# Performance work log

Measured on AMD Instinct MI355X. Metric: run time of the kernel, lower is better.

## Reference

```python
import jax, jax.numpy as jnp
import numpy as np

LN_EPS = 1e-5

def _ln(x, w, b):
    mu = jnp.mean(x, -1, keepdims=True)
    var = jnp.mean((x - mu) ** 2, -1, keepdims=True)
    return (x - mu) / jnp.sqrt(var + LN_EPS) * w + b

def _rot_fwd(x, c, s):
    dh = x.shape[-1] // 2
    r, i = x[..., :dh], x[..., dh:]
    return jnp.concatenate([r * c - i * s, r * s + i * c], axis=-1)

def _rot_inv(x, c, s):
    dh = x.shape[-1] // 2
    r, i = x[..., :dh], x[..., dh:]
    return jnp.concatenate([r * c + i * s, -r * s + i * c], axis=-1)

def _sheaf(x, thetas, alpha, corr_W):
    # causal offsets for window=3
    B, T, d = x.shape
    offsets = [-3, -2, -1, 0]
    lap = jnp.zeros_like(x)
    for idx, delta in enumerate(offsets):
        th = thetas[idx]
        c, s = jnp.cos(th), jnp.sin(th)
        Rx = _rot_fwd(x, c, s)
        if delta == 0:
            x_nb = x
        else:
            ad = -delta
            zeros = jnp.zeros((B, ad, d), dtype=x.dtype)
            x_nb = jnp.concatenate([zeros, x[:, :T - ad, :]], axis=1)
        lap = lap + _rot_inv(Rx - x_nb, c, s)
    out = x - jnp.abs(alpha) * lap
    return out + jnp.einsum('btd,od->bto', out, corr_W)

def _gist_rotation(x, gist_theta, gist_mag, gist_weights, gist_strength, ln_w, ln_b):
    # Scale-1 path: gist_weights present. theta: (B, dh)
    dh = x.shape[-1] // 2
    w = gist_weights[..., None] * gist_mag              # (B, K, 1)
    w = w / (jnp.sum(w, axis=1, keepdims=True) + 1e-8)
    theta = jnp.sum(w * gist_theta, axis=1)             # (B, dh)
    theta = theta * jax.nn.sigmoid(gist_strength)
    c = jnp.cos(theta)[:, None, :]                      # (B, 1, dh)
    s = jnp.sin(theta)[:, None, :]
    r, i = x[..., :dh], x[..., dh:]
    rot = jnp.concatenate([r * c - i * s, r * s + i * c], axis=-1)
    return _ln(rot, ln_w, ln_b)

def _gist_cross_attn(x, gist_theta, gist_mag, Wq, Wk, Wv, Wo, gist_up_W, gist_up_b, n_heads=16):
    B, T, d = x.shape
    K = gist_theta.shape[1]
    dh = d // n_heads
    gist_repr = jnp.einsum('bkf,of->bko', jnp.concatenate([gist_theta, gist_mag], axis=-1), gist_up_W) + gist_up_b  # (B,K,d)
    Q = jnp.einsum('btd,od->bto', x, Wq).reshape(B, T, n_heads, dh).transpose(0, 2, 1, 3)          # (B,H,T,dh)
    Kh = jnp.einsum('bkd,od->bko', gist_repr, Wk).reshape(B, K, n_heads, dh).transpose(0, 2, 1, 3)  # (B,H,K,dh)
    V = jnp.einsum('bkd,od->bko', gist_repr, Wv).reshape(B, K, n_heads, dh).transpose(0, 2, 1, 3)
    scores = jnp.einsum('bhtd,bhkd->bhtk', Q, Kh) / jnp.sqrt(jnp.asarray(dh, x.dtype))
    ctx = jnp.einsum('bhtk,bhkd->bhtd', jax.nn.softmax(scores, axis=-1), V)
    ctx = ctx.transpose(0, 2, 1, 3).reshape(B, T, d)
    return jnp.einsum('btd,od->bto', ctx, Wo)

def _forward(x, gist_theta, gist_mag, gist_weights,
             ln_sheaf_w, ln_sheaf_b, sheaf_thetas, alpha, corr_W,
             ln_gist_w, ln_gist_b, gist_strength, gr_ln_w, gr_ln_b,
             ln_gca_w, ln_gca_b, Wq, Wk, Wv, Wo, gist_up_W, gist_up_b):
    x = x + _sheaf(_ln(x, ln_sheaf_w, ln_sheaf_b), sheaf_thetas, alpha, corr_W)
    xn = _ln(x, ln_gist_w, ln_gist_b)
    x = x + (_gist_rotation(xn, gist_theta, gist_mag, gist_weights, gist_strength, gr_ln_w, gr_ln_b) - xn)
    x = x + _gist_cross_attn(_ln(x, ln_gca_w, ln_gca_b), gist_theta, gist_mag,
                             Wq, Wk, Wv, Wo, gist_up_W, gist_up_b)
    return x

def setup_inputs() -> dict:
    key = jax.random.key(0)
    ks = jax.random.split(key, 16)
    B, T, d, K = 4, 2048, 2048, 16
    dh = d // 2
    scale = 1.0 / np.sqrt(d)
    inp = {
        'x': jax.random.normal(ks[0], (B, T, d), jnp.float32),
        'gist_theta': jax.random.normal(ks[1], (B, K, dh), jnp.float32),
        'gist_mag': jax.random.uniform(ks[2], (B, K, 1), jnp.float32),
        'gist_weights': jax.random.uniform(ks[3], (B, K), jnp.float32),
        'ln_sheaf_w': jnp.ones((d,), jnp.float32),
        'ln_sheaf_b': jnp.zeros((d,), jnp.float32),
        'sheaf_thetas': 0.1 * jax.random.normal(ks[4], (4, dh), jnp.float32),
        'alpha': jnp.asarray(0.15, jnp.float32),
        'corr_W': scale * jax.random.normal(ks[5], (d, d), jnp.float32),
        'ln_gist_w': jnp.ones((d,), jnp.float32),
        'ln_gist_b': jnp.zeros((d,), jnp.float32),
        'gist_strength': jnp.asarray(0.0, jnp.float32),
        'gr_ln_w': jnp.ones((d,), jnp.float32),
        'gr_ln_b': jnp.zeros((d,), jnp.float32),
        'ln_gca_w': jnp.ones((d,), jnp.float32),
        'ln_gca_b': jnp.zeros((d,), jnp.float32),
        'Wq': scale * jax.random.normal(ks[6], (d, d), jnp.float32),
        'Wk': scale * jax.random.normal(ks[7], (d, d), jnp.float32),
        'Wv': scale * jax.random.normal(ks[8], (d, d), jnp.float32),
        'Wo': scale * jax.random.normal(ks[9], (d, d), jnp.float32),
        'gist_up_W': (1.0 / np.sqrt(dh + 1)) * jax.random.normal(ks[10], (d, dh + 1), jnp.float32),
        'gist_up_b': jnp.zeros((d,), jnp.float32),
    }
    return inp

def reference(x, gist_theta, gist_mag, gist_weights,
              ln_sheaf_w, ln_sheaf_b, sheaf_thetas, alpha, corr_W,
              ln_gist_w, ln_gist_b, gist_strength, gr_ln_w, gr_ln_b,
              ln_gca_w, ln_gca_b, Wq, Wk, Wv, Wo, gist_up_W, gist_up_b):
    return _forward(x, gist_theta, gist_mag, gist_weights,
                    ln_sheaf_w, ln_sheaf_b, sheaf_thetas, alpha, corr_W,
                    ln_gist_w, ln_gist_b, gist_strength, gr_ln_w, gr_ln_b,
                    ln_gca_w, ln_gca_b, Wq, Wk, Wv, Wo, gist_up_W, gist_up_b)
```

## Files before the change

kernel.cpp:

```cpp
#include <hip/hip_runtime.h>
#include <hip/hip_bf16.h>

typedef unsigned short u16;
typedef unsigned int   u32;

using frag_ab = __attribute__((ext_vector_type(8))) short;
using frag_cd = __attribute__((ext_vector_type(4))) float;

__device__ __forceinline__ float bf2f(u16 u) {
    union { u32 i; float f; } v; v.i = ((u32)u) << 16; return v.f;
}
__device__ __forceinline__ u16 f2bf(float f) {
    __hip_bfloat16 h = __float2bfloat16(f);
    u16 u; __builtin_memcpy(&u, &h, 2); return u;
}
__device__ __forceinline__ float lo2f(u32 u) { union { u32 i; float f; } v; v.i = u << 16; return v.f; }
__device__ __forceinline__ float hi2f(u32 u) { union { u32 i; float f; } v; v.i = u & 0xffff0000u; return v.f; }
__device__ __forceinline__ void unpack8(uint4 v, float* f) {
    f[0]=lo2f(v.x); f[1]=hi2f(v.x); f[2]=lo2f(v.y); f[3]=hi2f(v.y);
    f[4]=lo2f(v.z); f[5]=hi2f(v.z); f[6]=lo2f(v.w); f[7]=hi2f(v.w);
}
__device__ __forceinline__ void load4f(const u16* p, float* f) {
    ushort4 v = *reinterpret_cast<const ushort4*>(p);
    f[0]=bf2f(v.x); f[1]=bf2f(v.y); f[2]=bf2f(v.z); f[3]=bf2f(v.w);
}
__device__ __forceinline__ void store4bf(u16* p, const float* f) {
    ushort4 v; v.x=f2bf(f[0]); v.y=f2bf(f[1]); v.z=f2bf(f[2]); v.w=f2bf(f[3]);
    *reinterpret_cast<ushort4*>(p) = v;
}
__device__ __forceinline__ u32 pack2(float a, float b) {
    return (u32)f2bf(a) | ((u32)f2bf(b) << 16);
}

__device__ __forceinline__ void gld16(const u16* g, u16* l) {
    __builtin_amdgcn_global_load_lds(
        (const __attribute__((address_space(1))) u32*)g,
        (__attribute__((address_space(3))) u32*)l, 16, 0, 0);
}

__device__ __forceinline__ u32 ldsaddr(const u16* p) {
    return (u32)(uintptr_t)(const __attribute__((address_space(3))) u16*)p;
}

__device__ __forceinline__ frag_ab dsread16(u32 a) {
    frag_ab r;
    asm volatile("ds_read_b128 %0, %1" : "=v"(r) : "v"(a));
    return r;
}

__device__ __forceinline__ void block_reduce2(float& s, float& ss, float* red) {
    #pragma unroll
    for (int off = 32; off > 0; off >>= 1) {
        s  += __shfl_down(s, off, 64);
        ss += __shfl_down(ss, off, 64);
    }
    int wv = threadIdx.x >> 6, ln = threadIdx.x & 63;
    if (ln == 0) { red[wv*2] = s; red[wv*2+1] = ss; }
    __syncthreads();
    s  = red[0] + red[2] + red[4] + red[6];
    ss = red[1] + red[3] + red[5] + red[7];
    __syncthreads();
}

__global__ __launch_bounds__(256) void convert_kernel(
    const float* __restrict__ in, u16* __restrict__ out, int n4)
{
    int i = blockIdx.x * 256 + threadIdx.x;
    if (i < n4) {
        float4 v = reinterpret_cast<const float4*>(in)[i];
        ushort4 o; o.x=f2bf(v.x); o.y=f2bf(v.y); o.z=f2bf(v.z); o.w=f2bf(v.w);
        reinterpret_cast<ushort4*>(out)[i] = o;
    }
}

__global__ __launch_bounds__(256) void convert2_kernel(
    const float* __restrict__ s0, const float* __restrict__ s1,
    u16* __restrict__ d0, u16* __restrict__ d1, int n4)
{
    int i = blockIdx.x * 256 + threadIdx.x;
    if (i >= n4) return;
    const float* s = blockIdx.y ? s1 : s0;
    u16*         d = blockIdx.y ? d1 : d0;
    float4 v = reinterpret_cast<const float4*>(s)[i];
    ushort4 o; o.x=f2bf(v.x); o.y=f2bf(v.y); o.z=f2bf(v.z); o.w=f2bf(v.w);
    reinterpret_cast<ushort4*>(d)[i] = o;
}

__global__ __launch_bounds__(256) void convert3_kernel(
    const float* __restrict__ s0, const float* __restrict__ s1,
    const float* __restrict__ s2,
    u16* __restrict__ d0, u16* __restrict__ d1, u16* __restrict__ d2, int n4)
{
    int i = blockIdx.x * 256 + threadIdx.x;
    if (i >= n4) return;
    const float* s = blockIdx.y == 0 ? s0 : (blockIdx.y == 1 ? s1 : s2);
    u16*         d = blockIdx.y == 0 ? d0 : (blockIdx.y == 1 ? d1 : d2);
    float4 v = reinterpret_cast<const float4*>(s)[i];
    ushort4 o; o.x=f2bf(v.x); o.y=f2bf(v.y); o.z=f2bf(v.z); o.w=f2bf(v.w);
    reinterpret_cast<ushort4*>(d)[i] = o;
}

__global__ __launch_bounds__(256) void apad_kernel(
    const float* __restrict__ gth, const float* __restrict__ gmag,
    u16* __restrict__ Abuf)
{
    const int r = blockIdx.x;
    const int tid = threadIdx.x;
    for (int c0 = tid*4; c0 < 1056; c0 += 1024) {
        float f[4];
        #pragma unroll
        for (int i = 0; i < 4; ++i) {
            int c = c0 + i;
            f[i] = (c < 1024) ? gth[(size_t)r*1024 + c] : (c == 1024 ? gmag[r] : 0.f);
        }
        store4bf(Abuf + (size_t)r*1056 + c0, f);
    }
}

__global__ __launch_bounds__(256) void wpad_kernel(
    const float* __restrict__ upW, u16* __restrict__ Bbuf)
{
    const int r = blockIdx.x;
    const int tid = threadIdx.x;
    for (int c0 = tid*4; c0 < 1056; c0 += 1024) {
        float f[4];
        #pragma unroll
        for (int i = 0; i < 4; ++i) {
            int c = c0 + i;
            f[i] = (c < 1025) ? upW[(size_t)r*1025 + c] : 0.f;
        }
        store4bf(Bbuf + (size_t)r*1056 + c0, f);
    }
}

__global__ __launch_bounds__(256) void setup_kernel(
    const float* __restrict__ sheaf_th, const float* __restrict__ gth,
    const float* __restrict__ gmag, const float* __restrict__ gwts,
    const float* __restrict__ strength, float* __restrict__ sheaf_cs,
    float* __restrict__ gist_cs)
{
    int bx = blockIdx.x, tid = threadIdx.x;
    if (bx < 4) {
        for (int j = tid; j < 1024; j += 256) {
            float th = sheaf_th[bx*1024 + j];
            sheaf_cs[bx*1024 + j]        = cosf(th);
            sheaf_cs[4096 + bx*1024 + j] = sinf(th);
        }
    } else {
        int b = bx - 4;
        float w[16], wsum = 0.f;
        #pragma unroll
        for (int k = 0; k < 16; ++k) {
            w[k] = gwts[b*16+k] * gmag[b*16+k];
            wsum += w[k];
        }
        float inv = 1.f / (wsum + 1e-8f);
        float sig = 1.f / (1.f + expf(-strength[0]));
        for (int j = tid; j < 1024; j += 256) {
            float th = 0.f;
            #pragma unroll
            for (int k = 0; k < 16; ++k)
                th += w[k] * inv * gth[(size_t)(b*16+k)*1024 + j];
            th *= sig;
            gist_cs[b*1024 + j]        = cosf(th);
            gist_cs[4096 + b*1024 + j] = sinf(th);
        }
    }
}

__global__ __launch_bounds__(256) void ln_kernel(
    const float* __restrict__ in, const float* __restrict__ w,
    const float* __restrict__ b, u16* __restrict__ out)
{
    __shared__ float red[8];
    const size_t base = (size_t)blockIdx.x * 2048;
    const int e0 = threadIdx.x * 8;
    float x[8];
    *reinterpret_cast<float4*>(&x[0]) = *reinterpret_cast<const float4*>(in + base + e0);
    *reinterpret_cast<float4*>(&x[4]) = *reinterpret_cast<const float4*>(in + base + e0 + 4);
    float s = 0.f, ss = 0.f;
    #pragma unroll
    for (int i = 0; i < 8; ++i) { s += x[i]; ss += x[i]*x[i]; }
    block_reduce2(s, ss, red);
    const float mu = s * (1.f/2048.f);
    const float rin = rsqrtf(ss * (1.f/2048.f) - mu*mu + 1e-5f);
    float wv[8], bv[8];
    *reinterpret_cast<float4*>(&wv[0]) = *reinterpret_cast<const float4*>(w + e0);
    *reinterpret_cast<float4*>(&wv[4]) = *reinterpret_cast<const float4*>(w + e0 + 4);
    *reinterpret_cast<float4*>(&bv[0]) = *reinterpret_cast<const float4*>(b + e0);
    *reinterpret_cast<float4*>(&bv[4]) = *reinterpret_cast<const float4*>(b + e0 + 4);
    float o[8];
    #pragma unroll
    for (int i = 0; i < 8; ++i) o[i] = (x[i]-mu)*rin*wv[i] + bv[i];
    uint4 st = { pack2(o[0],o[1]), pack2(o[2],o[3]), pack2(o[4],o[5]), pack2(o[6],o[7]) };
    *reinterpret_cast<uint4*>(out + base + e0) = st;
}

__global__ __launch_bounds__(256) void sheaf_kernel(
    const u16* __restrict__ x1, const float* __restrict__ scs,
    const float* __restrict__ alpha_p, u16* __restrict__ pre)
{
    const int row = blockIdx.x;
    const int t = row & 2047;
    const int j0 = threadIdx.x * 4;
    const size_t base = (size_t)row * 2048;
    const float a = fabsf(alpha_p[0]);

    float xr[4], xi[4];
    load4f(x1 + base + j0, xr);
    load4f(x1 + base + 1024 + j0, xi);
    float lr[4], li[4];
    #pragma unroll
    for (int m = 0; m < 4; ++m) { lr[m] = 4.f*xr[m]; li[m] = 4.f*xi[m]; }

    #pragma unroll
    for (int idx = 0; idx < 4; ++idx) {
        const int sh = 3 - idx;
        if (t >= sh) {
            const float4 c4 = *reinterpret_cast<const float4*>(&scs[idx*1024 + j0]);
            const float4 s4 = *reinterpret_cast<const float4*>(&scs[4096 + idx*1024 + j0]);
            float c[4] = {c4.x, c4.y, c4.z, c4.w};
            float sn[4] = {s4.x, s4.y, s4.z, s4.w};
            float yr[4], yi[4];
            load4f(x1 + base - (size_t)sh*2048 + j0, yr);
            load4f(x1 + base - (size_t)sh*2048 + 1024 + j0, yi);
            #pragma unroll
            for (int m = 0; m < 4; ++m) {
                lr[m] -= yr[m]*c[m] + yi[m]*sn[m];
                li[m] -= yi[m]*c[m] - yr[m]*sn[m];
            }
        }
    }
    float pr[4], pi[4];
    #pragma unroll
    for (int m = 0; m < 4; ++m) { pr[m] = xr[m] - a*lr[m]; pi[m] = xi[m] - a*li[m]; }
    store4bf(pre + base + j0, pr);
    store4bf(pre + base + 1024 + j0, pi);
}

__global__ __launch_bounds__(256) void stage2_kernel(
    const u16* __restrict__ xA, const float* __restrict__ gcs,
    const float* __restrict__ lgw, const float* __restrict__ lgb,
    const float* __restrict__ grw, const float* __restrict__ grb,
    const float* __restrict__ gcaw, const float* __restrict__ gcab,
    u16* __restrict__ xB, u16* __restrict__ x2)
{
    __shared__ float red[8];
    const int row = blockIdx.x;
    const int b = row >> 11;
    const int j0 = threadIdx.x * 4;
    const size_t base = (size_t)row * 2048;

    float ar[4], ai[4];
    load4f(xA + base + j0, ar);
    load4f(xA + base + 1024 + j0, ai);

    float s = 0.f, ss = 0.f;
    #pragma unroll
    for (int m = 0; m < 4; ++m) { s += ar[m]+ai[m]; ss += ar[m]*ar[m] + ai[m]*ai[m]; }
    block_reduce2(s, ss, red);
    float mu = s * (1.f/2048.f);
    float rin = rsqrtf(ss * (1.f/2048.f) - mu*mu + 1e-5f);

    float w0[4], b0[4], w1[4], b1[4];
    *reinterpret_cast<float4*>(w0) = *reinterpret_cast<const float4*>(lgw + j0);
    *reinterpret_cast<float4*>(b0) = *reinterpret_cast<const float4*>(lgb + j0);
    *reinterpret_cast<float4*>(w1) = *reinterpret_cast<const float4*>(lgw + 1024 + j0);
    *reinterpret_cast<float4*>(b1) = *reinterpret_cast<const float4*>(lgb + 1024 + j0);
    float xnr[4], xni[4];
    #pragma unroll
    for (int m = 0; m < 4; ++m) {
        xnr[m] = (ar[m]-mu)*rin*w0[m] + b0[m];
        xni[m] = (ai[m]-mu)*rin*w1[m] + b1[m];
    }

    const float4 c4 = *reinterpret_cast<const float4*>(&gcs[b*1024 + j0]);
    const float4 s4 = *reinterpret_cast<const float4*>(&gcs[4096 + b*1024 + j0]);
    float c[4] = {c4.x, c4.y, c4.z, c4.w};
    float sn[4] = {s4.x, s4.y, s4.z, s4.w};
    float rr[4], ri[4];
    #pragma unroll
    for (int m = 0; m < 4; ++m) {
        rr[m] = xnr[m]*c[m] - xni[m]*sn[m];
        ri[m] = xnr[m]*sn[m] + xni[m]*c[m];
    }

    s = 0.f; ss = 0.f;
    #pragma unroll
    for (int m = 0; m < 4; ++m) { s += rr[m]+ri[m]; ss += rr[m]*rr[m] + ri[m]*ri[m]; }
    block_reduce2(s, ss, red);
    float mu2 = s * (1.f/2048.f);
    float rin2 = rsqrtf(ss * (1.f/2048.f) - mu2*mu2 + 1e-5f);

    *reinterpret_cast<float4*>(w0) = *reinterpret_cast<const float4*>(grw + j0);
    *reinterpret_cast<float4*>(b0) = *reinterpret_cast<const float4*>(grb + j0);
    *reinterpret_cast<float4*>(w1) = *reinterpret_cast<const float4*>(grw + 1024 + j0);
    *reinterpret_cast<float4*>(b1) = *reinterpret_cast<const float4*>(grb + 1024 + j0);
    float br[4], bi[4];
    #pragma unroll
    for (int m = 0; m < 4; ++m) {
        float gr_ = (rr[m]-mu2)*rin2*w0[m] + b0[m];
        float gi_ = (ri[m]-mu2)*rin2*w1[m] + b1[m];
        br[m] = ar[m] - xnr[m] + gr_;
        bi[m] = ai[m] - xni[m] + gi_;
    }
    store4bf(xB + base + j0, br);
    store4bf(xB + base + 1024 + j0, bi);

    s = 0.f; ss = 0.f;
    #pragma unroll
    for (int m = 0; m < 4; ++m) { s += br[m]+bi[m]; ss += br[m]*br[m] + bi[m]*bi[m]; }
    block_reduce2(s, ss, red);
    float mu3 = s * (1.f/2048.f);
    float rin3 = rsqrtf(ss * (1.f/2048.f) - mu3*mu3 + 1e-5f);

    *reinterpret_cast<float4*>(w0) = *reinterpret_cast<const float4*>(gcaw + j0);
    *reinterpret_cast<float4*>(b0) = *reinterpret_cast<const float4*>(gcab + j0);
    *reinterpret_cast<float4*>(w1) = *reinterpret_cast<const float4*>(gcaw + 1024 + j0);
    *reinterpret_cast<float4*>(b1) = *reinterpret_cast<const float4*>(gcab + 1024 + j0);
    float o0[4], o1[4];
    #pragma unroll
    for (int m = 0; m < 4; ++m) {
        o0[m] = (br[m]-mu3)*rin3*w0[m] + b0[m];
        o1[m] = (bi[m]-mu3)*rin3*w1[m] + b1[m];
    }
    store4bf(x2 + base + j0, o0);
    store4bf(x2 + base + 1024 + j0, o1);
}

__global__ __launch_bounds__(256) void attn_kernel(
    const u16* __restrict__ Q, const u16* __restrict__ KV,
    u16* __restrict__ ctx)
{
    const int wv = threadIdx.x >> 6;
    const int lane = threadIdx.x & 63;
    const int tg = blockIdx.x * 4 + wv;
    const int b = tg >> 11;
    const size_t base = (size_t)tg * 2048 + lane * 32;

    float q[32];
    #pragma unroll
    for (int c = 0; c < 4; ++c)
        unpack8(*reinterpret_cast<const uint4*>(Q + base + c*8), &q[c*8]);

    float sc[16];
    #pragma unroll
    for (int k = 0; k < 16; ++k) {
        const u16* kr = KV + (size_t)(b*16 + k) * 4096 + lane*32;
        float p = 0.f;
        #pragma unroll
        for (int c = 0; c < 4; ++c) {
            float kv8[8]; unpack8(*reinterpret_cast<const uint4*>(kr + c*8), kv8);
            #pragma unroll
            for (int e = 0; e < 8; ++e) p += q[c*8+e] * kv8[e];
        }
        sc[k] = p;
    }
    #pragma unroll
    for (int k = 0; k < 16; ++k) {
        sc[k] += __shfl_xor(sc[k], 1, 64);
        sc[k] += __shfl_xor(sc[k], 2, 64);
        sc[k] *= 0.08838834764831845f;
    }
    float m = sc[0];
    #pragma unroll
    for (int k = 1; k < 16; ++k) m = fmaxf(m, sc[k]);
    float sum = 0.f;
    #pragma unroll
    for (int k = 0; k < 16; ++k) { sc[k] = expf(sc[k]-m); sum += sc[k]; }
    const float inv = 1.f / sum;

    float o[32];
    #pragma unroll
    for (int e = 0; e < 32; ++e) o[e] = 0.f;
    #pragma unroll
    for (int k = 0; k < 16; ++k) {
        const float p = sc[k] * inv;
        const u16* vr = KV + (size_t)(b*16 + k) * 4096 + 2048 + lane*32;
        #pragma unroll
        for (int c = 0; c < 4; ++c) {
            float v8[8]; unpack8(*reinterpret_cast<const uint4*>(vr + c*8), v8);
            #pragma unroll
            for (int e = 0; e < 8; ++e) o[c*8+e] += p * v8[e];
        }
    }
    #pragma unroll
    for (int c = 0; c < 4; ++c) {
        uint4 st = { pack2(o[c*8+0],o[c*8+1]), pack2(o[c*8+2],o[c*8+3]),
                     pack2(o[c*8+4],o[c*8+5]), pack2(o[c*8+6],o[c*8+7]) };
        *reinterpret_cast<uint4*>(ctx + base + c*8) = st;
    }
}

#define BM 128
#define BN 128
#define BK 32

template<int OUTMODE>
__global__ __launch_bounds__(256, 4) void gemm_bt_kernel(
    const u16* __restrict__ A, const u16* __restrict__ B,
    void* __restrict__ Cv, const float* __restrict__ addf,
    const u16* __restrict__ addb, const float* __restrict__ biasN,
    int M, int N, int K)
{
    __shared__ u16 As[2][8*512];
    __shared__ u16 Bs[2][8*512];

    const int tid = threadIdx.x;
    const int lane = tid & 63;
    const int wave = tid >> 6;
    const int wm = wave >> 1;
    const int wn = wave & 1;
    const int row0 = blockIdx.y * BM;
    const int col0 = blockIdx.x * BN;

    frag_cd acc[4][4] = {};

    const int srow   = lane >> 2;
    const int schunk = (lane & 3) ^ ((lane >> 3) & 3);
    const int scol   = schunk * 8;
    const int s0 = wave, s1 = wave + 4;

    int ra0 = row0 + s0*16 + srow; if (ra0 >= M) ra0 = M - 1;
    int ra1 = row0 + s1*16 + srow; if (ra1 >= M) ra1 = M - 1;
    const u16* gA0 = A + (size_t)ra0 * K + scol;
    const u16* gA1 = A + (size_t)ra1 * K + scol;
    const u16* gB0 = B + (size_t)(col0 + s0*16 + srow) * K + scol;
    const u16* gB1 = B + (size_t)(col0 + s1*16 + srow) * K + scol;

    const int fr = lane & 15;
    const int fq8 = lane >> 4;
    const int fslot = (4*fr + (fq8 ^ ((fr >> 1) & 3))) * 8;

    const int nsteps = K / BK;
    int ts = 0, te = nsteps;
    if (OUTMODE == 2) {
        ts = (nsteps * (int)blockIdx.z) / (int)gridDim.z;
        te = (nsteps * ((int)blockIdx.z + 1)) / (int)gridDim.z;
    }

    gld16(gA0 + ts*BK, &As[0][s0*512]);
    gld16(gA1 + ts*BK, &As[0][s1*512]);
    gld16(gB0 + ts*BK, &Bs[0][s0*512]);
    gld16(gB1 + ts*BK, &Bs[0][s1*512]);
    __syncthreads();

    int cur = 0;
    for (int t = ts; t < te; ++t) {
        if (t + 1 < te) {
            const int kt = (t + 1) * BK;
            gld16(gA0 + kt, &As[cur^1][s0*512]);
            gld16(gA1 + kt, &As[cur^1][s1*512]);
            gld16(gB0 + kt, &Bs[cur^1][s0*512]);
            gld16(gB1 + kt, &Bs[cur^1][s1*512]);
        }

        frag_ab af[4], bf_[4];
        #pragma unroll
        for (int i = 0; i < 4; ++i)
            af[i] = *reinterpret_cast<const frag_ab*>(&As[cur][(wm*4 + i)*512 + fslot]);
        #pragma unroll
        for (int j = 0; j < 4; ++j)
            bf_[j] = *reinterpret_cast<const frag_ab*>(&Bs[cur][(wn*4 + j)*512 + fslot]);
        #pragma unroll
        for (int i = 0; i < 4; ++i)
            #pragma unroll
            for (int j = 0; j < 4; ++j)
                acc[i][j] = __builtin_amdgcn_mfma_f32_16x16x32_bf16(af[i], bf_[j], acc[i][j], 0, 0, 0);

        __syncthreads();
        cur ^= 1;
    }

    float* Pz = (OUTMODE == 2)
        ? reinterpret_cast<float*>(Cv) + (size_t)blockIdx.z * M * N : nullptr;

    #pragma unroll
    for (int i = 0; i < 4; ++i) {
        #pragma unroll
        for (int j = 0; j < 4; ++j) {
            #pragma unroll
            for (int r = 0; r < 4; ++r) {
                const int grow = row0 + wm*64 + i*16 + (lane >> 4) * 4 + r;
                const int gcol = col0 + wn*64 + j*16 + (lane & 15);
                if (grow < M) {
                    const size_t idx = (size_t)grow * N + gcol;
                    float v = acc[i][j][r];
                    if (OUTMODE == 2) {
                        Pz[idx] = v;
                    } else {
                        if (addf) v += addf[idx];
                        if (addb) v += bf2f(addb[idx]);
                        if (biasN) v += biasN[gcol];
                        if (OUTMODE == 1) reinterpret_cast<float*>(Cv)[idx] = v;
                        else              reinterpret_cast<u16*>(Cv)[idx] = f2bf(v);
                    }
                }
            }
        }
    }
}

__global__ __launch_bounds__(256) void ksum_kernel(
    const float* __restrict__ part, int nz, int n4, int N,
    const float* __restrict__ biasN, u16* __restrict__ out)
{
    int i = blockIdx.x * 256 + threadIdx.x;
    if (i >= n4) return;
    const float4* p4 = reinterpret_cast<const float4*>(part);
    float4 s = p4[i];
    for (int z = 1; z < nz; ++z) {
        float4 t = p4[i + (size_t)z * n4];
        s.x += t.x; s.y += t.y; s.z += t.z; s.w += t.w;
    }
    if (biasN) {
        int col = (i * 4) % N;
        s.x += biasN[col]; s.y += biasN[col+1]; s.z += biasN[col+2]; s.w += biasN[col+3];
    }
    ushort4 o; o.x=f2bf(s.x); o.y=f2bf(s.y); o.z=f2bf(s.z); o.w=f2bf(s.w);
    reinterpret_cast<ushort4*>(out)[i] = o;
}

template<int OUTF32>
__global__ __launch_bounds__(512, 2) void gemm256_kernel(
    const u16* __restrict__ A, const u16* __restrict__ B,
    void* __restrict__ Cv, const float* __restrict__ addf,
    const u16* __restrict__ addb, const float* __restrict__ biasN,
    int M, int N, int K)
{
    extern __shared__ u16 lds[];
    u16* Abase = lds;
    u16* Bbase = lds + 32768;

    const int tid  = threadIdx.x;
    const int lane = tid & 63;
    const int wave = tid >> 6;
    const int wm   = wave >> 2;
    const int wn   = wave & 3;

    int id = (int)(blockIdx.y * gridDim.x + blockIdx.x);
    {
        const int nwg = (int)(gridDim.x * gridDim.y);
        if ((nwg & 7) == 0) id = (id & 7) * (nwg >> 3) + (id >> 3);
    }
    const int bx = id % (int)gridDim.x;
    const int by = id / (int)gridDim.x;
    const int row0 = by * 256;
    const int col0 = bx * 256;

    const int srow = lane >> 2;
    const int scol = ((lane & 3) ^ ((lane >> 3) & 3)) * 8;

    const u16* pA = A + (size_t)(row0 + wave*16 + srow) * K + scol;
    const u16* pB = B + (size_t)(col0 + wave*16 + srow) * K + scol;
    const size_t h128 = (size_t)128 * K;

    const int ldsW = wave * 1024;

    const int fr = lane & 15;
    const int fq8 = lane >> 4;
    const int fByte = (4*fr + (fq8 ^ ((fr >> 1) & 3))) * 16;

    const u32 uA = ldsaddr(Abase) + (u32)(wm * 16384) + (u32)fByte;
    const u32 uB = ldsaddr(Bbase) + (u32)((wn >> 1) * 16384 + (wn & 1) * 8192) + (u32)fByte;

    frag_cd acc[8][4] = {};
    frag_ab bfr[4][2];
    frag_ab afr[2][2];

#define STAGE256(SRC, DSTOFF, KT)                                   \
    gld16((SRC) + (KT),      (DSTOFF) + ldsW);                      \
    gld16((SRC) + (KT) + 32, (DSTOFF) + ldsW + 512);

    STAGE256(pB,        Bbase + 0*8192, 0);
    STAGE256(pB + h128, Bbase + 1*8192, 0);
    STAGE256(pA,        Abase + 0*8192, 0);
    STAGE256(pA + h128, Abase + 1*8192, 0);
    STAGE256(pB,        Bbase + 2*8192, 64);
    STAGE256(pB + h128, Bbase + 3*8192, 64);
    asm volatile("s_waitcnt vmcnt(4)" ::: "memory");
    __builtin_amdgcn_s_barrier();

    const int NI = K >> 7;
    for (int i = 0; i < NI; ++i) {
        const int t1k = i*128 + 64;
        int t2k = i*128 + 128; if (t2k >= K) t2k = K - 64;
        int t3k = i*128 + 192; if (t3k >= K) t3k = K - 64;

        #pragma unroll
        for (int p = 0; p < 8; ++p) {
            const int q = p & 3;
            const int bufc = p >> 2;

            if (q == 0) {
                #pragma unroll
                for (int n = 0; n < 4; ++n)
                    #pragma unroll
                    for (int ks = 0; ks < 2; ++ks)
                        bfr[n][ks] = dsread16(uB + (u32)(bufc*32768 + (n*2 + ks)*1024));
            }
            #pragma unroll
            for (int r = 0; r < 2; ++r)
                #pragma unroll
                for (int ks = 0; ks < 2; ++ks)
                    afr[r][ks] = dsread16(uA + (u32)(bufc*32768 + ((2*q + r)*2 + ks)*1024));

            switch (p) {
                case 0: STAGE256(pA,        Abase + 2*8192, t1k); break;
                case 1: STAGE256(pA + h128, Abase + 3*8192, t1k); break;
                case 2: STAGE256(pB,        Bbase + 0*8192, t2k); break;
                case 3: STAGE256(pB + h128, Bbase + 1*8192, t2k); break;
                case 4: STAGE256(pA,        Abase + 0*8192, t2k); break;
                case 5: STAGE256(pA + h128, Abase + 1*8192, t2k); break;
                case 6: STAGE256(pB,        Bbase + 2*8192, t3k); break;
                case 7: STAGE256(pB + h128, Bbase + 3*8192, t3k); break;
            }
            if (q == 0) asm volatile("s_waitcnt lgkmcnt(8)" ::: "memory");
            if (q == 3) asm volatile("s_waitcnt vmcnt(4)" ::: "memory");
            __builtin_amdgcn_s_barrier();
            asm volatile("s_waitcnt lgkmcnt(0)" ::: "memory");
            __builtin_amdgcn_sched_barrier(0);

            __builtin_amdgcn_s_setprio(1);
            #pragma unroll
            for (int ks = 0; ks < 2; ++ks)
                #pragma unroll
                for (int r = 0; r < 2; ++r)
                    #pragma unroll
                    for (int n = 0; n < 4; ++n)
                        acc[2*q + r][n] = __builtin_amdgcn_mfma_f32_16x16x32_bf16(
                            afr[r][ks], bfr[n][ks], acc[2*q + r][n], 0, 0, 0);
            __builtin_amdgcn_s_setprio(0);
            __builtin_amdgcn_s_barrier();
        }
    }
    asm volatile("s_waitcnt vmcnt(0)" ::: "memory");
#undef STAGE256

    #pragma unroll
    for (int m = 0; m < 8; ++m) {
        #pragma unroll
        for (int n = 0; n < 4; ++n) {
            #pragma unroll
            for (int r = 0; r < 4; ++r) {
                const int grow = row0 + wm*128 + m*16 + (lane >> 4) * 4 + r;
                const int gcol = col0 + wn*64 + n*16 + (lane & 15);
                const size_t idx = (size_t)grow * N + gcol;
                float v = acc[m][n][r];
                if (addf) v += addf[idx];
                if (addb) v += bf2f(addb[idx]);
                if (biasN) v += biasN[gcol];
                if (OUTF32) reinterpret_cast<float*>(Cv)[idx] = v;
                else        reinterpret_cast<u16*>(Cv)[idx] = f2bf(v);
            }
        }
    }
}

extern "C" void kernel_launch(void* const* d_in, const int* in_sizes, int n_in,
                              void* d_out, int out_size, void* d_ws, size_t ws_size,
                              hipStream_t stream)
{
    const float* x          = (const float*)d_in[0];
    const float* gist_theta = (const float*)d_in[1];
    const float* gist_mag   = (const float*)d_in[2];
    const float* gist_wts   = (const float*)d_in[3];
    const float* ln_sheaf_w = (const float*)d_in[4];
    const float* ln_sheaf_b = (const float*)d_in[5];
    const float* sheaf_th   = (const float*)d_in[6];
    const float* alpha      = (const float*)d_in[7];
    const float* corr_W     = (const float*)d_in[8];
    const float* ln_gist_w  = (const float*)d_in[9];
    const float* ln_gist_b  = (const float*)d_in[10];
    const float* strength   = (const float*)d_in[11];
    const float* gr_w       = (const float*)d_in[12];
    const float* gr_b       = (const float*)d_in[13];
    const float* gca_w      = (const float*)d_in[14];
    const float* gca_b      = (const float*)d_in[15];
    const float* Wq         = (const float*)d_in[16];
    const float* Wk         = (const float*)d_in[17];
    const float* Wv         = (const float*)d_in[18];
    const float* Wo         = (const float*)d_in[19];
    const float* up_W       = (const float*)d_in[20];
    const float* up_b       = (const float*)d_in[21];
    float* out = (float*)d_out;

    static bool attr_done = false;
    if (!attr_done) {
        hipFuncSetAttribute((const void*)&gemm256_kernel<0>,
                            hipFuncAttributeMaxDynamicSharedMemorySize, 131072);
        hipFuncSetAttribute((const void*)&gemm256_kernel<1>,
                            hipFuncAttributeMaxDynamicSharedMemorySize, 131072);
        attr_done = true;
    }

    char* w = (char*)d_ws;
    const size_t BIG = (size_t)4 * 2048 * 2048 * sizeof(u16);
    u16* wA = (u16*)(w);
    u16* wB = (u16*)(w + BIG);
    u16* wC = (u16*)(w + 2*BIG);
    u16* wslot = (u16*)(w + 3*BIG);
    char* small = w + 3*BIG + (size_t)2048*2048*sizeof(u16);
    float* sheaf_cs = (float*)(small);
    float* gist_cs  = (float*)(small + 32768);
    u16* repr = (u16*)(small + 65536);
    u16* KV   = repr + 64*2048;
    float* part = (float*)((char*)KV + (size_t)64*4096*sizeof(u16));
    const size_t part_bytes = (size_t)8 * 64 * 4096 * sizeof(float);
    char* after_part = (char*)part + part_bytes;
    const bool ksplit = ws_size >= (size_t)(after_part - w);

    u16* wslot2 = (u16*)after_part;
    u16* wslot3 = wslot2 + (size_t)2048*2048;
    const bool roomy = ws_size >= (size_t)((char*)(wslot3 + (size_t)2048*2048) - w);

    const int W4 = 2048*2048/4;
    const dim3 gBig256(2048/256, 8192/256), gKV(32, 1), gRepr(16, 1);

    setup_kernel<<<8, 256, 0, stream>>>(sheaf_th, gist_theta, gist_mag, gist_wts,
                                        strength, sheaf_cs, gist_cs);

    if (roomy) {
        convert3_kernel<<<dim3(4096,3), 256, 0, stream>>>(corr_W, Wq, Wo,
                                                          wslot, wslot2, wslot3, W4);
    }
    convert2_kernel<<<dim3(4096,2), 256, 0, stream>>>(Wk, Wv,
                                                      wB, wB + (size_t)2048*2048, W4);

    apad_kernel<<<64, 256, 0, stream>>>(gist_theta, gist_mag, wC);
    wpad_kernel<<<2048, 256, 0, stream>>>(up_W, roomy ? (u16*)((char*)wslot3 + (size_t)2048*2048*2) : wslot);
    const bool padroom = ws_size >= (size_t)((char*)(wslot3 + (size_t)2048*2048) - w)
                         + (size_t)2048*1056*sizeof(u16);
    u16* padbuf = (roomy && padroom) ? (u16*)((char*)(wslot3 + (size_t)2048*2048)) : wslot;

    if (ksplit) {
        gemm_bt_kernel<2><<<dim3(16,1,4), 256, 0, stream>>>(wC, padbuf, part,
                                                 nullptr, nullptr, nullptr, 64, 2048, 1056);
        ksum_kernel<<<(64*2048/4 + 255)/256, 256, 0, stream>>>(part, 4, 64*2048/4, 2048,
                                                 up_b, repr);
    } else {
        gemm_bt_kernel<0><<<gRepr, 256, 0, stream>>>(wC, padbuf, repr, nullptr, nullptr, up_b,
                                                     64, 2048, 1056);
    }

    if (ksplit) {
        gemm_bt_kernel<2><<<dim3(32,1,8), 256, 0, stream>>>(repr, wB, part,
                                                 nullptr, nullptr, nullptr, 64, 4096, 2048);
        ksum_kernel<<<(64*4096/4 + 255)/256, 256, 0, stream>>>(part, 8, 64*4096/4, 4096,
                                                 nullptr, KV);
    } else {
        gemm_bt_kernel<0><<<gKV, 256, 0, stream>>>(repr, wB, KV, nullptr, nullptr, nullptr,
                                                   64, 4096, 2048);
    }

    ln_kernel<<<8192, 256, 0, stream>>>(x, ln_sheaf_w, ln_sheaf_b, wA);
    sheaf_kernel<<<8192, 256, 0, stream>>>(wA, sheaf_cs, alpha, wB);

    if (!roomy || padbuf == wslot)
        convert_kernel<<<4096, 256, 0, stream>>>(corr_W, wslot, W4);
    gemm256_kernel<0><<<gBig256, 512, 131072, stream>>>(wB, wslot, wA, x, wB, nullptr,
                                                8192, 2048, 2048);
    stage2_kernel<<<8192, 256, 0, stream>>>(wA, gist_cs, ln_gist_w, ln_gist_b,
                                            gr_w, gr_b, gca_w, gca_b,
                                            wC, wA);
    u16* qslot = roomy ? wslot2 : wslot;
    if (!roomy)
        convert_kernel<<<4096, 256, 0, stream>>>(Wq, wslot, W4);
    gemm256_kernel<0><<<gBig256, 512, 131072, stream>>>(wA, qslot, wB, nullptr, nullptr, nullptr,
                                                8192, 2048, 2048);
    attn_kernel<<<2048, 256, 0, stream>>>(wB, KV, wA);
    u16* oslot = roomy ? wslot3 : wslot;
    if (!roomy)
        convert_kernel<<<4096, 256, 0, stream>>>(Wo, wslot, W4);
    gemm256_kernel<1><<<gBig256, 512, 131072, stream>>>(wA, oslot, (void*)out, nullptr, wC, nullptr,
                                                8192, 2048, 2048);
}
```

Baseline: 633.2 us.

## Replace 256x256 pipelined GEMM with simpler 128x128 double-buffered GEMM

Swaps the 512-thread, 256x256-tile GEMM, which used 128 KB of dynamic LDS, a hand-scheduled multi-stage global-to-LDS pipeline and raw ds_read asm, for a 256-thread, 128x128-tile kernel. The new kernel uses static LDS double buffering with one __syncthreads per 64-wide K step. Smaller tiles quadruple the grid and drop the dynamic-LDS attribute setup, which may improve occupancy and load balance. In exchange, each tile reuses loaded data less and loses the fine-grained overlap of loads with MFMA work. It also sends the wpad output straight to padbuf so the padded up-projection weights land where the following GEMM reads them.

```diff
diff --git a/kernel.cpp b/kernel.cpp
--- a/kernel.cpp
+++ b/kernel.cpp
@@ -36,16 +36,6 @@
     __builtin_amdgcn_global_load_lds(
         (const __attribute__((address_space(1))) u32*)g,
         (__attribute__((address_space(3))) u32*)l, 16, 0, 0);
-}
-
-__device__ __forceinline__ u32 ldsaddr(const u16* p) {
-    return (u32)(uintptr_t)(const __attribute__((address_space(3))) u16*)p;
-}
-
-__device__ __forceinline__ frag_ab dsread16(u32 a) {
-    frag_ab r;
-    asm volatile("ds_read_b128 %0, %1" : "=v"(r) : "v"(a));
-    return r;
 }
 
 __device__ __forceinline__ void block_reduce2(float& s, float& ss, float* red) {
@@ -522,131 +512,101 @@
 }
 
 template<int OUTF32>
-__global__ __launch_bounds__(512, 2) void gemm256_kernel(
+__global__ __launch_bounds__(256, 2) void gemm_big_kernel(
     const u16* __restrict__ A, const u16* __restrict__ B,
     void* __restrict__ Cv, const float* __restrict__ addf,
     const u16* __restrict__ addb, const float* __restrict__ biasN,
     int M, int N, int K)
 {
-    extern __shared__ u16 lds[];
-    u16* Abase = lds;
-    u16* Bbase = lds + 32768;
+    __shared__ u16 As[2][16*512];
+    __shared__ u16 Bs[2][16*512];
 
     const int tid  = threadIdx.x;
     const int lane = tid & 63;
     const int wave = tid >> 6;
-    const int wm   = wave >> 2;
-    const int wn   = wave & 3;
+    const int wm   = wave >> 1;
+    const int wn   = wave & 1;
 
     int id = (int)(blockIdx.y * gridDim.x + blockIdx.x);
     {
         const int nwg = (int)(gridDim.x * gridDim.y);
         if ((nwg & 7) == 0) id = (id & 7) * (nwg >> 3) + (id >> 3);
     }
-    const int bx = id % (int)gridDim.x;
-    const int by = id / (int)gridDim.x;
-    const int row0 = by * 256;
-    const int col0 = bx * 256;
+    const int row0 = (id / (int)gridDim.x) * BM;
+    const int col0 = (id % (int)gridDim.x) * BN;
+
+    frag_cd acc[4][4] = {};
 
     const int srow = lane >> 2;
     const int scol = ((lane & 3) ^ ((lane >> 3) & 3)) * 8;
-
-    const u16* pA = A + (size_t)(row0 + wave*16 + srow) * K + scol;
-    const u16* pB = B + (size_t)(col0 + wave*16 + srow) * K + scol;
-    const size_t h128 = (size_t)128 * K;
-
-    const int ldsW = wave * 1024;
+    const int s0 = wave, s1 = wave + 4;
+
+    const u16* gA0 = A + (size_t)(row0 + s0*16 + srow) * K + scol;
+    const u16* gA1 = A + (size_t)(row0 + s1*16 + srow) * K + scol;
+    const u16* gB0 = B + (size_t)(col0 + s0*16 + srow) * K + scol;
+    const u16* gB1 = B + (size_t)(col0 + s1*16 + srow) * K + scol;
 
     const int fr = lane & 15;
     const int fq8 = lane >> 4;
-    const int fByte = (4*fr + (fq8 ^ ((fr >> 1) & 3))) * 16;
-
-    const u32 uA = ldsaddr(Abase) + (u32)(wm * 16384) + (u32)fByte;
-    const u32 uB = ldsaddr(Bbase) + (u32)((wn >> 1) * 16384 + (wn & 1) * 8192) + (u32)fByte;
-
-    frag_cd acc[8][4] = {};
-    frag_ab bfr[4][2];
-    frag_ab afr[2][2];
-
-#define STAGE256(SRC, DSTOFF, KT)                                   \
-    gld16((SRC) + (KT),      (DSTOFF) + ldsW);                      \
-    gld16((SRC) + (KT) + 32, (DSTOFF) + ldsW + 512);
-
-    STAGE256(pB,        Bbase + 0*8192, 0);
-    STAGE256(pB + h128, Bbase + 1*8192, 0);
-    STAGE256(pA,        Abase + 0*8192, 0);
-    STAGE256(pA + h128, Abase + 1*8192, 0);
-    STAGE256(pB,        Bbase + 2*8192, 64);
-    STAGE256(pB + h128, Bbase + 3*8192, 64);
-    asm volatile("s_waitcnt vmcnt(4)" ::: "memory");
-    __builtin_amdgcn_s_barrier();
-
-    const int NI = K >> 7;
-    for (int i = 0; i < NI; ++i) {
-        const int t1k = i*128 + 64;
-        int t2k = i*128 + 128; if (t2k >= K) t2k = K - 64;
-        int t3k = i*128 + 192; if (t3k >= K) t3k = K - 64;
-
-        #pragma unroll
-        for (int p = 0; p < 8; ++p) {
-            const int q = p & 3;
-            const int bufc = p >> 2;
-
-            if (q == 0) {
+    const int fslot = (4*fr + (fq8 ^ ((fr >> 1) & 3))) * 8;
+
+    const int nt = K >> 6;
+
+#define STAGEBIG(BUF, KT)                                           \
+    gld16(gA0 + (KT),      &As[BUF][(s0*2+0)*512]);                 \
+    gld16(gA0 + (KT) + 32, &As[BUF][(s0*2+1)*512]);                 \
+    gld16(gA1 + (KT),      &As[BUF][(s1*2+0)*512]);                 \
+    gld16(gA1 + (KT) + 32, &As[BUF][(s1*2+1)*512]);                 \
+    gld16(gB0 + (KT),      &Bs[BUF][(s0*2+0)*512]);                 \
+    gld16(gB0 + (KT) + 32, &Bs[BUF][(s0*2+1)*512]);                 \
+    gld16(gB1 + (KT),      &Bs[BUF][(s1*2+0)*512]);                 \
+    gld16(gB1 + (KT) + 32, &Bs[BUF][(s1*2+1)*512]);
+
+    STAGEBIG(0, 0);
+    __syncthreads();
+
+    int cur = 0;
+    for (int t = 0; t < nt; ++t) {
+        if (t + 1 < nt) {
+            const int kt = (t + 1) << 6;
+            if (cur) { STAGEBIG(0, kt); } else { STAGEBIG(1, kt); }
+        }
+
+        frag_ab bf_[4][2];
+        #pragma unroll
+        for (int j = 0; j < 4; ++j)
+            #pragma unroll
+            for (int ks = 0; ks < 2; ++ks)
+                bf_[j][ks] = *reinterpret_cast<const frag_ab*>(
+                    &Bs[cur][((wn*4 + j)*2 + ks)*512 + fslot]);
+
+        #pragma unroll
+        for (int ks = 0; ks < 2; ++ks)
+            #pragma unroll
+            for (int i = 0; i < 4; ++i) {
+                frag_ab af = *reinterpret_cast<const frag_ab*>(
+                    &As[cur][((wm*4 + i)*2 + ks)*512 + fslot]);
                 #pragma unroll
-                for (int n = 0; n < 4; ++n)
-                    #pragma unroll
-                    for (int ks = 0; ks < 2; ++ks)
-                        bfr[n][ks] = dsread16(uB + (u32)(bufc*32768 + (n*2 + ks)*1024));
+                for (int j = 0; j < 4; ++j)
+                    acc[i][j] = __builtin_amdgcn_mfma_f32_16x16x32_bf16(
+                        af, bf_[j][ks], acc[i][j], 0, 0, 0);
             }
-            #pragma unroll
-            for (int r = 0; r < 2; ++r)
-                #pragma unroll
-                for (int ks = 0; ks < 2; ++ks)
-                    afr[r][ks] = dsread16(uA + (u32)(bufc*32768 + ((2*q + r)*2 + ks)*1024));
-
-            switch (p) {
-                case 0: STAGE256(pA,        Abase + 2*8192, t1k); break;
-                case 1: STAGE256(pA + h128, Abase + 3*8192, t1k); break;
-                case 2: STAGE256(pB,        Bbase + 0*8192, t2k); break;
-                case 3: STAGE256(pB + h128, Bbase + 1*8192, t2k); break;
-                case 4: STAGE256(pA,        Abase + 0*8192, t2k); break;
-                case 5: STAGE256(pA + h128, Abase + 1*8192, t2k); break;
-                case 6: STAGE256(pB,        Bbase + 2*8192, t3k); break;
-                case 7: STAGE256(pB + h128, Bbase + 3*8192, t3k); break;
-            }
-            if (q == 0) asm volatile("s_waitcnt lgkmcnt(8)" ::: "memory");
-            if (q == 3) asm volatile("s_waitcnt vmcnt(4)" ::: "memory");
-            __builtin_amdgcn_s_barrier();
-            asm volatile("s_waitcnt lgkmcnt(0)" ::: "memory");
-            __builtin_amdgcn_sched_barrier(0);
-
-            __builtin_amdgcn_s_setprio(1);
-            #pragma unroll
-            for (int ks = 0; ks < 2; ++ks)
-                #pragma unroll
-                for (int r = 0; r < 2; ++r)
-                    #pragma unroll
-                    for (int n = 0; n < 4; ++n)
-                        acc[2*q + r][n] = __builtin_amdgcn_mfma_f32_16x16x32_bf16(
-                            afr[r][ks], bfr[n][ks], acc[2*q + r][n], 0, 0, 0);
-            __builtin_amdgcn_s_setprio(0);
-            __builtin_amdgcn_s_barrier();
-        }
-    }
-    asm volatile("s_waitcnt vmcnt(0)" ::: "memory");
-#undef STAGE256
-
-    #pragma unroll
-    for (int m = 0; m < 8; ++m) {
-        #pragma unroll
-        for (int n = 0; n < 4; ++n) {
+
+        __syncthreads();
+        cur ^= 1;
+    }
+#undef STAGEBIG
+
+    #pragma unroll
+    for (int i = 0; i < 4; ++i) {
+        #pragma unroll
+        for (int j = 0; j < 4; ++j) {
             #pragma unroll
             for (int r = 0; r < 4; ++r) {
-                const int grow = row0 + wm*128 + m*16 + (lane >> 4) * 4 + r;
-                const int gcol = col0 + wn*64 + n*16 + (lane & 15);
+                const int grow = row0 + wm*64 + i*16 + (lane >> 4) * 4 + r;
+                const int gcol = col0 + wn*64 + j*16 + (lane & 15);
                 const size_t idx = (size_t)grow * N + gcol;
-                float v = acc[m][n][r];
+                float v = acc[i][j][r];
                 if (addf) v += addf[idx];
                 if (addb) v += bf2f(addb[idx]);
                 if (biasN) v += biasN[gcol];
@@ -685,15 +645,6 @@
     const float* up_b       = (const float*)d_in[21];
     float* out = (float*)d_out;
 
-    static bool attr_done = false;
-    if (!attr_done) {
-        hipFuncSetAttribute((const void*)&gemm256_kernel<0>,
-                            hipFuncAttributeMaxDynamicSharedMemorySize, 131072);
-        hipFuncSetAttribute((const void*)&gemm256_kernel<1>,
-                            hipFuncAttributeMaxDynamicSharedMemorySize, 131072);
-        attr_done = true;
-    }
-
     char* w = (char*)d_ws;
     const size_t BIG = (size_t)4 * 2048 * 2048 * sizeof(u16);
     u16* wA = (u16*)(w);
@@ -715,7 +666,7 @@
     const bool roomy = ws_size >= (size_t)((char*)(wslot3 + (size_t)2048*2048) - w);
 
     const int W4 = 2048*2048/4;
-    const dim3 gBig256(2048/256, 8192/256), gKV(32, 1), gRepr(16, 1);
+    const dim3 gBig(2048/128, 8192/128), gKV(32, 1), gRepr(16, 1);
 
     setup_kernel<<<8, 256, 0, stream>>>(sheaf_th, gist_theta, gist_mag, gist_wts,
                                         strength, sheaf_cs, gist_cs);
@@ -728,10 +679,10 @@
                                                       wB, wB + (size_t)2048*2048, W4);
 
     apad_kernel<<<64, 256, 0, stream>>>(gist_theta, gist_mag, wC);
-    wpad_kernel<<<2048, 256, 0, stream>>>(up_W, roomy ? (u16*)((char*)wslot3 + (size_t)2048*2048*2) : wslot);
     const bool padroom = ws_size >= (size_t)((char*)(wslot3 + (size_t)2048*2048) - w)
                          + (size_t)2048*1056*sizeof(u16);
     u16* padbuf = (roomy && padroom) ? (u16*)((char*)(wslot3 + (size_t)2048*2048)) : wslot;
+    wpad_kernel<<<2048, 256, 0, stream>>>(up_W, padbuf);
 
     if (ksplit) {
         gemm_bt_kernel<2><<<dim3(16,1,4), 256, 0, stream>>>(wC, padbuf, part,
@@ -758,20 +709,20 @@
 
     if (!roomy || padbuf == wslot)
         convert_kernel<<<4096, 256, 0, stream>>>(corr_W, wslot, W4);
-    gemm256_kernel<0><<<gBig256, 512, 131072, stream>>>(wB, wslot, wA, x, wB, nullptr,
-                                                8192, 2048, 2048);
+    gemm_big_kernel<0><<<gBig, 256, 0, stream>>>(wB, wslot, wA, x, wB, nullptr,
+                                                 8192, 2048, 2048);
     stage2_kernel<<<8192, 256, 0, stream>>>(wA, gist_cs, ln_gist_w, ln_gist_b,
                                             gr_w, gr_b, gca_w, gca_b,
                                             wC, wA);
     u16* qslot = roomy ? wslot2 : wslot;
     if (!roomy)
         convert_kernel<<<4096, 256, 0, stream>>>(Wq, wslot, W4);
-    gemm256_kernel<0><<<gBig256, 512, 131072, stream>>>(wA, qslot, wB, nullptr, nullptr, nullptr,
-                                                8192, 2048, 2048);
+    gemm_big_kernel<0><<<gBig, 256, 0, stream>>>(wA, qslot, wB, nullptr, nullptr, nullptr,
+                                                 8192, 2048, 2048);
     attn_kernel<<<2048, 256, 0, stream>>>(wB, KV, wA);
     u16* oslot = roomy ? wslot3 : wslot;
     if (!roomy)
         convert_kernel<<<4096, 256, 0, stream>>>(Wo, wslot, W4);
-    gemm256_kernel<1><<<gBig256, 512, 131072, stream>>>(wA, oslot, (void*)out, nullptr, wC, nullptr,
-                                                8192, 2048, 2048);
-}
+    gemm_big_kernel<1><<<gBig, 256, 0, stream>>>(wA, oslot, (void*)out, nullptr, wC, nullptr,
+                                                 8192, 2048, 2048);
+}
```

Measured after the change: 657.1 us. +3.8%, slower.
